# Optimization experiments

Measured on AMD Instinct MI355X. Metric: run time of the kernel, lower is better.

Reference implementation:

```python
import jax, jax.numpy as jnp
import numpy as np

B, F0, K = 256, 40, 32          # batch, num fields, embedding dim
CIN_SIZE = [200, 200]            # layer widths (field_num[1:])


def setup_inputs() -> dict:
    key = jax.random.key(0)
    ks = jax.random.split(key, 1 + 4 * len(CIN_SIZE))
    field_num = [F0] + CIN_SIZE
    d = {"inputs": jax.random.normal(ks[0], (B, F0, K), dtype=jnp.float32)}
    for i in range(len(CIN_SIZE)):
        # W_query: (1, Fi, K); W_key/W_value: (1, F0, K); cin_W: (1, F0*Fi, F_{i+1})
        d[f"wq{i}"] = jax.random.normal(ks[1 + 4 * i], (1, field_num[i], K), dtype=jnp.float32) * 0.05
        d[f"wk{i}"] = jax.random.normal(ks[2 + 4 * i], (1, F0, K), dtype=jnp.float32) * 0.05
        d[f"wv{i}"] = jax.random.normal(ks[3 + 4 * i], (1, F0, K), dtype=jnp.float32) * 0.05
        lim = (6.0 / (F0 * field_num[i] + field_num[i + 1])) ** 0.5  # glorot uniform
        d[f"cw{i}"] = jax.random.uniform(ks[4 + 4 * i], (1, F0 * field_num[i], field_num[i + 1]),
                                         minval=-lim, maxval=lim, dtype=jnp.float32)
    return d


def _cin(inputs, params):
    # inputs: [B, F0, K]; params: list of (wq, wk, wv, cw) per CIN layer
    Bb, F0_, Kk = inputs.shape
    res = inputs
    outs = []
    for (wq, wk, wv, cw) in params:
        x0_wk = inputs * wk                 # [B, F0, K]
        x0_wv = inputs * wv                 # [B, F0, K]
        xi_wq = res * wq                    # [B, Fi, K]
        # per-embedding-slot outer product scores: phi[b,k,f0,fi]
        phi = jnp.einsum('bfk,bgk->bkfg', x0_wk, xi_wq)
        # exp + normalize over F0 axis == softmax over axis=2
        alpha = jax.nn.softmax(phi, axis=2)                      # [B, K, F0, Fi]
        x = alpha * jnp.transpose(x0_wv, (0, 2, 1))[:, :, :, None]  # [B, K, F0, Fi]
        x = x.reshape(Bb, Kk, -1)           # flatten (f0, fi) row-major -> f0*Fi + fi
        # conv1d with kernel width 1 == channel matmul: [B, K, F0*Fi] @ [F0*Fi, F_{i+1}]
        out = jnp.einsum('bkc,cj->bjk', x, cw[0])                # [B, F_{i+1}, K]
        outs.append(out)
        res = out
    cat = jnp.concatenate(outs, axis=1)     # [B, sum(cin_size), K]
    return cat.sum(axis=-1)                 # [B, sum(cin_size)]


def reference(inputs, wq0, wk0, wv0, cw0, wq1, wk1, wv1, cw1):
    return _cin(inputs, [(wq0, wk0, wv0, cw0), (wq1, wk1, wv1, cw1)])
```

## Files before the change

kernel.cpp:

```cpp
#include <hip/hip_runtime.h>
#include <hip/hip_bf16.h>


#define NF0  40
#define KD   32
#define NJ   200
#define NTHR 512
#define G0   120
#define G1   600

typedef short bf16x8 __attribute__((ext_vector_type(8)));
typedef float f32x16 __attribute__((ext_vector_type(16)));
typedef unsigned short u16;
typedef unsigned int   u32;

static __device__ __forceinline__ u16 f2bf(float f) {
    __hip_bfloat16 h = __float2bfloat16(f);
    return *reinterpret_cast<u16*>(&h);
}

template<int FI>
__global__ __launch_bounds__(256)
void pack_b(const float* __restrict__ cw, u16* __restrict__ bp) {
    __shared__ u16 s[48][33];
    const int fi = blockIdx.x, nt = blockIdx.y;
    const int t = threadIdx.x;
    for (int idx = t; idx < 48 * 32; idx += 256) {
        int f0 = idx >> 5, jj = idx & 31, j = nt * 32 + jj;
        float v = (f0 < NF0 && j < NJ) ? cw[(size_t)(f0 * FI + fi) * NJ + j] : 0.f;
        s[f0][jj] = f2bf(v);
    }
    __syncthreads();
    if (t < 192) {
        const int g = t >> 6, l = t & 63;
        u16 v[8];
        #pragma unroll
        for (int i = 0; i < 8; ++i) v[i] = s[g * 16 + 8 * (l >> 5) + i][l & 31];
        constexpr int G = FI * 3;
        *reinterpret_cast<bf16x8*>(bp + ((size_t)(nt * G + fi * 3 + g) * 64 + l) * 8)
            = *reinterpret_cast<const bf16x8*>(v);
    }
}

__global__ __launch_bounds__(NTHR, 2)
void cin_fused(const float* __restrict__ x0,
               const float* __restrict__ wq0, const float* __restrict__ wk0,
               const float* __restrict__ wv0,
               const float* __restrict__ wq1, const float* __restrict__ wk1,
               const float* __restrict__ wv1,
               const u16* __restrict__ bp0, const u16* __restrict__ bp1,
               float* __restrict__ out) {
    __shared__ float s_res[NJ][33];
    __shared__ float s_o1[224];
    const int tid = threadIdx.x, b = blockIdx.x;
    const int wid = tid >> 6, lane = tid & 63;
    const int sk = lane & 31, sh = lane >> 5;
    const bool hb = (lane >= 32);

    for (int i = tid; i < NJ * 33; i += NTHR) (&s_res[0][0])[i] = 0.f;
    if (tid < 224) s_o1[tid] = 0.f;

    float xkr[24], xvr[24];
    f32x16 acc[7];

    auto load_xw = [&](const float* wk, const float* wv) {
        #pragma unroll
        for (int m = 0; m < 24; ++m) {
            const int f0 = sh * 24 + m;
            if (f0 < NF0) {
                const float v = x0[(size_t)b * 1280 + f0 * 32 + sk];
                xkr[m] = v * wk[f0 * 32 + sk];
                xvr[m] = v * wv[f0 * 32 + sk];
            } else { xkr[m] = 0.f; xvr[m] = 0.f; }
        }
    };
    auto zacc = [&]() {
        #pragma unroll
        for (int nt = 0; nt < 7; ++nt)
            #pragma unroll
            for (int r = 0; r < 16; ++r) acc[nt][r] = 0.f;
    };

    auto do_fi = [&](float q, const u16* __restrict__ bp, int G, int g0) {
        float e[24], d = 0.f;
        #pragma unroll
        for (int m = 0; m < 24; ++m) { e[m] = __expf(xkr[m] * q); d += e[m]; }
        if (sh) d -= 8.0f;
        d += __shfl_xor(d, 32);
        const float r = 1.0f / d;
        u32 pk[12];
        #pragma unroll
        for (int p = 0; p < 12; ++p)
            pk[p] = (u32)f2bf(e[2*p] * r * xvr[2*p])
                  | ((u32)f2bf(e[2*p+1] * r * xvr[2*p+1]) << 16);
        u32 tmp[4];
        #pragma unroll
        for (int j = 0; j < 4; ++j) tmp[j] = (u32)__shfl_xor((int)pk[4 + j], 32);
        #pragma unroll
        for (int s = 0; s < 3; ++s) {
            u32 a4[4];
            #pragma unroll
            for (int j = 0; j < 4; ++j)
                a4[j] = (s == 0) ? (hb ? tmp[j] : pk[j])
                      : (s == 1) ? (hb ? pk[j] : pk[8 + j])
                                 : (hb ? pk[8 + j] : tmp[j]);
            bf16x8 av;
            __builtin_memcpy(&av, a4, 16);
            const u16* bgp = bp + ((size_t)(g0 + s) * 64 + lane) * 8;
            #pragma unroll
            for (int nt = 0; nt < 7; ++nt) {
                bf16x8 bv = *reinterpret_cast<const bf16x8*>(bgp + (size_t)nt * G * 512);
                acc[nt] = __builtin_amdgcn_mfma_f32_32x32x16_bf16(av, bv, acc[nt], 0, 0, 0);
            }
        }
    };

    load_xw(wk0, wv0);
    zacc();
    for (int t = 0; t < 5; ++t) {
        const int fi = wid + t * 8;
        const float q = x0[(size_t)b * 1280 + fi * 32 + sk] * wq0[fi * 32 + sk];
        do_fi(q, bp0, G0, fi * 3);
    }
    __syncthreads();
    #pragma unroll
    for (int nt = 0; nt < 7; ++nt) {
        const int j = nt * 32 + sk;
        if (j < NJ) {
            #pragma unroll
            for (int r = 0; r < 16; ++r) {
                const int k = (r & 3) + 8 * (r >> 2) + 4 * sh;
                atomicAdd(&s_res[j][k], acc[nt][r]);
            }
        }
    }
    __syncthreads();

    if (tid < NJ) {
        float s = 0.f;
        #pragma unroll
        for (int k = 0; k < 32; ++k) s += s_res[tid][k];
        out[(size_t)b * 400 + tid] = s;
    }

    load_xw(wk1, wv1);
    zacc();
    for (int t = 0; t < 25; ++t) {
        const int fi = wid + t * 8;
        const float q = s_res[fi][sk] * wq1[fi * 32 + sk];
        do_fi(q, bp1, G1, fi * 3);
    }
    #pragma unroll
    for (int nt = 0; nt < 7; ++nt) {
        float s = 0.f;
        #pragma unroll
        for (int r = 0; r < 16; ++r) s += acc[nt][r];
        s += __shfl_xor(s, 32);
        const int j = nt * 32 + sk;
        if (!hb && j < NJ) atomicAdd(&s_o1[j], s);
    }
    __syncthreads();
    if (tid < NJ) out[(size_t)b * 400 + 200 + tid] = s_o1[tid];
}

extern "C" void kernel_launch(void* const* d_in, const int* in_sizes, int n_in,
                              void* d_out, int out_size, void* d_ws, size_t ws_size,
                              hipStream_t stream) {
    const float* x0  = (const float*)d_in[0];
    const float* wq0 = (const float*)d_in[1];
    const float* wk0 = (const float*)d_in[2];
    const float* wv0 = (const float*)d_in[3];
    const float* cw0 = (const float*)d_in[4];
    const float* wq1 = (const float*)d_in[5];
    const float* wk1 = (const float*)d_in[6];
    const float* wv1 = (const float*)d_in[7];
    const float* cw1 = (const float*)d_in[8];
    float* out = (float*)d_out;

    char* ws = (char*)d_ws;
    u16* bp0 = (u16*)ws;
    u16* bp1 = (u16*)(ws + 860160);

    pack_b<40> <<<dim3(40, 7),  256, 0, stream>>>(cw0, bp0);
    pack_b<200><<<dim3(200, 7), 256, 0, stream>>>(cw1, bp1);

    cin_fused<<<256, NTHR, 0, stream>>>(x0, wq0, wk0, wv0,
                                        wq1, wk1, wv1, bp0, bp1, out);
}
```

Measured before the change: 220.4 us.

## Split fused CIN kernel into per-layer kernels with finer grid partitioning

Replaces the single per-batch fused kernel (256 blocks of 512 threads) with two per-layer kernels. Each splits the output-column tiles in half, and layer 1 also splits the fi range in half, giving 512 and 1024 blocks of 256 threads. The intermediate result goes through a global workspace and is reduced with global atomics into a zeroed output. Each wave now holds 4 accumulator tiles instead of 7, which frees registers for higher occupancy, and B-fragment loads are issued ahead of the softmax math. In exchange it adds an extra launch, a memset, global round-trips for the intermediate, and nondeterministic atomic summation order.

```diff
diff --git a/kernel.cpp b/kernel.cpp
--- a/kernel.cpp
+++ b/kernel.cpp
@@ -2,12 +2,8 @@
 #include <hip/hip_bf16.h>
 
 
-#define NF0  40
-#define KD   32
-#define NJ   200
-#define NTHR 512
-#define G0   120
-#define G1   600
+#define NF0 40
+#define NJ  200
 
 typedef short bf16x8 __attribute__((ext_vector_type(8)));
 typedef float f32x16 __attribute__((ext_vector_type(16)));
@@ -42,125 +38,172 @@
     }
 }
 
-__global__ __launch_bounds__(NTHR, 2)
-void cin_fused(const float* __restrict__ x0,
-               const float* __restrict__ wq0, const float* __restrict__ wk0,
-               const float* __restrict__ wv0,
-               const float* __restrict__ wq1, const float* __restrict__ wk1,
-               const float* __restrict__ wv1,
-               const u16* __restrict__ bp0, const u16* __restrict__ bp1,
-               float* __restrict__ out) {
-    __shared__ float s_res[NJ][33];
-    __shared__ float s_o1[224];
-    const int tid = threadIdx.x, b = blockIdx.x;
+template<int LAYER>
+__global__ __launch_bounds__(256, 3)
+void cin_layer(const float* __restrict__ x0,
+               const float* __restrict__ wq, const float* __restrict__ wk,
+               const float* __restrict__ wv,
+               const u16* __restrict__ bp,
+               float* __restrict__ res,
+               float* __restrict__ out)
+{
+    constexpr int FI   = LAYER ? 200 : 40;
+    constexpr int G    = FI * 3;
+    constexpr int NFIW = LAYER ? 25 : 10;
+
+    extern __shared__ float smem[];
+    float* s_xk  = smem;
+    float* s_xv  = smem + 1536;
+    float* s_o   = smem + 3072;
+    float* s_res = smem + 3200;
+
+    const int bid = blockIdx.x;
+    const int xx = bid & 7;
+    int b, jh, fi0;
+    if constexpr (LAYER == 0) {
+        jh = xx >> 2; fi0 = 0;
+        b = (bid >> 3) * 4 + (xx & 3);
+    } else {
+        jh = xx >> 2; fi0 = ((xx >> 1) & 1) * 100;
+        b = (bid >> 3) + ((xx & 1) << 7);
+    }
+    const int NT = jh ? 3 : 4;
+    const int ntbase = jh * 4;
+
+    const int tid = threadIdx.x;
     const int wid = tid >> 6, lane = tid & 63;
-    const int sk = lane & 31, sh = lane >> 5;
-    const bool hb = (lane >= 32);
-
-    for (int i = tid; i < NJ * 33; i += NTHR) (&s_res[0][0])[i] = 0.f;
-    if (tid < 224) s_o1[tid] = 0.f;
-
-    float xkr[24], xvr[24];
-    f32x16 acc[7];
-
-    auto load_xw = [&](const float* wk, const float* wv) {
+    const int sk = lane & 31, h = lane >> 5;
+
+    if (tid < 128) s_o[tid] = 0.f;
+    if constexpr (LAYER == 0)
+        for (int i = tid; i < 128 * 33; i += 256) s_res[i] = 0.f;
+
+    for (int i = tid; i < 1536; i += 256) {
+        const int r = i >> 5, k = i & 31;
+        float xk = 0.f, xv = 0.f;
+        if (r < NF0) {
+            const float v = x0[(size_t)b * 1280 + r * 32 + k];
+            xk = v * wk[r * 32 + k];
+            xv = v * wv[r * 32 + k];
+        }
+        s_xk[i] = xk;
+        s_xv[i] = xv;
+    }
+    __syncthreads();
+
+    const int fw0 = fi0 + wid * NFIW;
+
+    f32x16 acc[4];
+    #pragma unroll
+    for (int n = 0; n < 4; ++n)
+        #pragma unroll
+        for (int r = 0; r < 16; ++r) acc[n][r] = 0.f;
+
+    const u16* bb[4];
+    #pragma unroll
+    for (int n = 0; n < 4; ++n) {
+        const int nt = ntbase + ((n < 3) ? n : (NT - 1));
+        bb[n] = bp + (((size_t)nt * G + fw0 * 3) * 64 + lane) * 8;
+    }
+
+    for (int t = 0; t < NFIW; ++t) {
+        const int fi = fw0 + t;
+        bf16x8 v0[4], v1[4], v2[4];
+        #pragma unroll
+        for (int n = 0; n < 4; ++n) v0[n] = *reinterpret_cast<const bf16x8*>(bb[n]);
+        #pragma unroll
+        for (int n = 0; n < 4; ++n) v1[n] = *reinterpret_cast<const bf16x8*>(bb[n] + 512);
+        #pragma unroll
+        for (int n = 0; n < 4; ++n) v2[n] = *reinterpret_cast<const bf16x8*>(bb[n] + 1024);
+
+        float qin;
+        if constexpr (LAYER == 0) qin = x0[(size_t)b * 1280 + fi * 32 + sk];
+        else                      qin = res[(size_t)b * 6400 + fi * 32 + sk];
+        const float q = qin * wq[fi * 32 + sk];
+
+        float e[24], d = 0.f;
         #pragma unroll
         for (int m = 0; m < 24; ++m) {
-            const int f0 = sh * 24 + m;
-            if (f0 < NF0) {
-                const float v = x0[(size_t)b * 1280 + f0 * 32 + sk];
-                xkr[m] = v * wk[f0 * 32 + sk];
-                xvr[m] = v * wv[f0 * 32 + sk];
-            } else { xkr[m] = 0.f; xvr[m] = 0.f; }
-        }
-    };
-    auto zacc = [&]() {
-        #pragma unroll
-        for (int nt = 0; nt < 7; ++nt)
-            #pragma unroll
-            for (int r = 0; r < 16; ++r) acc[nt][r] = 0.f;
-    };
-
-    auto do_fi = [&](float q, const u16* __restrict__ bp, int G, int g0) {
-        float e[24], d = 0.f;
-        #pragma unroll
-        for (int m = 0; m < 24; ++m) { e[m] = __expf(xkr[m] * q); d += e[m]; }
-        if (sh) d -= 8.0f;
+            const int row = 16 * (m >> 3) + 8 * h + (m & 7);
+            e[m] = __expf(s_xk[row * 32 + sk] * q);
+            d += e[m];
+        }
+        if (h) d -= 8.0f;
         d += __shfl_xor(d, 32);
-        const float r = 1.0f / d;
+        float rcp;
+        asm("v_rcp_f32 %0, %1" : "=v"(rcp) : "v"(d));
+
         u32 pk[12];
         #pragma unroll
-        for (int p = 0; p < 12; ++p)
-            pk[p] = (u32)f2bf(e[2*p] * r * xvr[2*p])
-                  | ((u32)f2bf(e[2*p+1] * r * xvr[2*p+1]) << 16);
-        u32 tmp[4];
-        #pragma unroll
-        for (int j = 0; j < 4; ++j) tmp[j] = (u32)__shfl_xor((int)pk[4 + j], 32);
-        #pragma unroll
-        for (int s = 0; s < 3; ++s) {
-            u32 a4[4];
-            #pragma unroll
-            for (int j = 0; j < 4; ++j)
-                a4[j] = (s == 0) ? (hb ? tmp[j] : pk[j])
-                      : (s == 1) ? (hb ? pk[j] : pk[8 + j])
-                                 : (hb ? pk[8 + j] : tmp[j]);
-            bf16x8 av;
-            __builtin_memcpy(&av, a4, 16);
-            const u16* bgp = bp + ((size_t)(g0 + s) * 64 + lane) * 8;
-            #pragma unroll
-            for (int nt = 0; nt < 7; ++nt) {
-                bf16x8 bv = *reinterpret_cast<const bf16x8*>(bgp + (size_t)nt * G * 512);
-                acc[nt] = __builtin_amdgcn_mfma_f32_32x32x16_bf16(av, bv, acc[nt], 0, 0, 0);
+        for (int p = 0; p < 12; ++p) {
+            const int m0 = (p >> 2) * 8 + (p & 3) * 2;
+            const int row0 = 16 * (p >> 2) + 8 * h + (p & 3) * 2;
+            const float y0 = e[m0]     * rcp * s_xv[row0 * 32 + sk];
+            const float y1 = e[m0 + 1] * rcp * s_xv[(row0 + 1) * 32 + sk];
+            pk[p] = (u32)f2bf(y0) | ((u32)f2bf(y1) << 16);
+        }
+        bf16x8 A0, A1, A2;
+        __builtin_memcpy(&A0, &pk[0], 16);
+        __builtin_memcpy(&A1, &pk[4], 16);
+        __builtin_memcpy(&A2, &pk[8], 16);
+
+        #pragma unroll
+        for (int n = 0; n < 4; ++n)
+            acc[n] = __builtin_amdgcn_mfma_f32_32x32x16_bf16(A0, v0[n], acc[n], 0, 0, 0);
+        #pragma unroll
+        for (int n = 0; n < 4; ++n)
+            acc[n] = __builtin_amdgcn_mfma_f32_32x32x16_bf16(A1, v1[n], acc[n], 0, 0, 0);
+        #pragma unroll
+        for (int n = 0; n < 4; ++n)
+            acc[n] = __builtin_amdgcn_mfma_f32_32x32x16_bf16(A2, v2[n], acc[n], 0, 0, 0);
+
+        #pragma unroll
+        for (int n = 0; n < 4; ++n) bb[n] += 1536;
+    }
+
+    if constexpr (LAYER == 0) {
+        #pragma unroll
+        for (int n = 0; n < 4; ++n) {
+            if (n < NT) {
+                #pragma unroll
+                for (int r = 0; r < 16; ++r) {
+                    const int k = (r & 3) + 8 * (r >> 2) + 4 * h;
+                    atomicAdd(&s_res[(n * 32 + sk) * 33 + k], acc[n][r]);
+                }
             }
         }
-    };
-
-    load_xw(wk0, wv0);
-    zacc();
-    for (int t = 0; t < 5; ++t) {
-        const int fi = wid + t * 8;
-        const float q = x0[(size_t)b * 1280 + fi * 32 + sk] * wq0[fi * 32 + sk];
-        do_fi(q, bp0, G0, fi * 3);
-    }
-    __syncthreads();
-    #pragma unroll
-    for (int nt = 0; nt < 7; ++nt) {
-        const int j = nt * 32 + sk;
-        if (j < NJ) {
-            #pragma unroll
-            for (int r = 0; r < 16; ++r) {
-                const int k = (r & 3) + 8 * (r >> 2) + 4 * sh;
-                atomicAdd(&s_res[j][k], acc[nt][r]);
+        __syncthreads();
+        for (int i = tid; i < NT * 32 * 32; i += 256) {
+            const int jl = i >> 5, k = i & 31;
+            const int j = ntbase * 32 + jl;
+            if (j < NJ) res[(size_t)b * 6400 + j * 32 + k] = s_res[jl * 33 + k];
+        }
+        if (tid < NT * 32) {
+            const int j = ntbase * 32 + tid;
+            if (j < NJ) {
+                float s = 0.f;
+                #pragma unroll
+                for (int k = 0; k < 32; ++k) s += s_res[tid * 33 + k];
+                out[(size_t)b * 400 + j] = s;
             }
         }
-    }
-    __syncthreads();
-
-    if (tid < NJ) {
-        float s = 0.f;
-        #pragma unroll
-        for (int k = 0; k < 32; ++k) s += s_res[tid][k];
-        out[(size_t)b * 400 + tid] = s;
-    }
-
-    load_xw(wk1, wv1);
-    zacc();
-    for (int t = 0; t < 25; ++t) {
-        const int fi = wid + t * 8;
-        const float q = s_res[fi][sk] * wq1[fi * 32 + sk];
-        do_fi(q, bp1, G1, fi * 3);
-    }
-    #pragma unroll
-    for (int nt = 0; nt < 7; ++nt) {
-        float s = 0.f;
-        #pragma unroll
-        for (int r = 0; r < 16; ++r) s += acc[nt][r];
-        s += __shfl_xor(s, 32);
-        const int j = nt * 32 + sk;
-        if (!hb && j < NJ) atomicAdd(&s_o1[j], s);
-    }
-    __syncthreads();
-    if (tid < NJ) out[(size_t)b * 400 + 200 + tid] = s_o1[tid];
+    } else {
+        #pragma unroll
+        for (int n = 0; n < 4; ++n) {
+            if (n < NT) {
+                float s = 0.f;
+                #pragma unroll
+                for (int r = 0; r < 16; ++r) s += acc[n][r];
+                s += __shfl_xor(s, 32);
+                if (h == 0) atomicAdd(&s_o[n * 32 + sk], s);
+            }
+        }
+        __syncthreads();
+        if (tid < NT * 32) {
+            const int j = ntbase * 32 + tid;
+            if (j < NJ) atomicAdd(&out[(size_t)b * 400 + 200 + j], s_o[tid]);
+        }
+    }
 }
 
 extern "C" void kernel_launch(void* const* d_in, const int* in_sizes, int n_in,
@@ -178,12 +221,17 @@
     float* out = (float*)d_out;
 
     char* ws = (char*)d_ws;
-    u16* bp0 = (u16*)ws;
-    u16* bp1 = (u16*)(ws + 860160);
+    float* res = (float*)ws;
+    u16* bp0 = (u16*)(ws + 6553600);
+    u16* bp1 = (u16*)(ws + 6553600 + 860160);
+
+    hipMemsetAsync(d_out, 0, (size_t)out_size * 4, stream);
 
     pack_b<40> <<<dim3(40, 7),  256, 0, stream>>>(cw0, bp0);
     pack_b<200><<<dim3(200, 7), 256, 0, stream>>>(cw1, bp1);
 
-    cin_fused<<<256, NTHR, 0, stream>>>(x0, wq0, wk0, wv0,
-                                        wq1, wk1, wv1, bp0, bp1, out);
-}
+    cin_layer<0><<<512,  256, (3200 + 128 * 33) * 4, stream>>>(
+        x0, wq0, wk0, wv0, bp0, res, out);
+    cin_layer<1><<<1024, 256, 3200 * 4, stream>>>(
+        x0, wq1, wk1, wv1, bp1, res, out);
+}
```

New measurement: 267.3 us. 21.3% more time.
